# Kernel optimization log

Measured on AMD Instinct MI355X. Metric: run time of the kernel, lower is better.

## Reference

```python
import jax, jax.numpy as jnp
import numpy as np

N = 100000
E = 3200000
NFEAT = 256
NHID = 128
NCLASS = 40
SCALE = 1.0


def setup_inputs() -> dict:
    key = jax.random.key(0)
    ks = jax.random.split(key, 8)
    x = jax.random.normal(ks[0], (N, NFEAT), dtype=jnp.float32)
    adj_row = jnp.sort(jax.random.randint(ks[1], (E,), 0, N, dtype=jnp.int32))
    adj_col = jax.random.randint(ks[2], (E,), 0, N, dtype=jnp.int32)
    adj_val = jax.random.uniform(ks[3], (E,), dtype=jnp.float32)
    # parameters (reset_parameters: weight ~ N(0,1), bias ~ N(-1,1) -> normal with mean -1? no:
    # bias.normal_(-stdv, stdv) with stdv=1 means mean=-1, std=1)
    W1 = jax.random.normal(ks[4], (NFEAT, NHID), dtype=jnp.float32)
    b1 = jax.random.normal(ks[5], (NHID,), dtype=jnp.float32) - 1.0
    W2 = jax.random.normal(ks[6], (NHID, NCLASS), dtype=jnp.float32)
    b2 = jax.random.normal(ks[7], (NCLASS,), dtype=jnp.float32) - 1.0
    return {"x": x, "adj_row": adj_row, "adj_col": adj_col, "adj_val": adj_val,
            "i": 0, "W1": W1, "b1": b1, "W2": W2, "b2": b2}


def spmm(row, col, val, dense):
    # adj @ dense where adj is sparse COO [N, N]
    gathered = val[:, None] * dense[col]          # [E, D]
    return jax.ops.segment_sum(gathered, row, num_segments=N)


def reference(x, adj_row, adj_col, adj_val, i, W1, b1, W2, b2):
    # layer 1: support = x @ W1; out = adj @ support + b1
    h = spmm(adj_row, adj_col, adj_val, x @ W1) + b1
    h = jax.nn.relu(h) * SCALE
    # dropout is identity (eval mode / training=False)
    # layer 2
    logits = spmm(adj_row, adj_col, adj_val, h @ W2) + b2
    return jax.nn.log_softmax(logits, axis=1)
```

## Files before the change

### kernel.cpp

```cpp
#include <hip/hip_runtime.h>
#include <hip/hip_bf16.h>
#include <math.h>


#define GCN_NFEAT 256
#define GCN_NHID  128
#define GCN_NCLASS 40
#define SUP2_LD   64

typedef __bf16 bf16_t;
typedef bf16_t bf16x8 __attribute__((ext_vector_type(8)));
typedef float  f32x4  __attribute__((ext_vector_type(4)));

static __device__ __forceinline__ unsigned short f2b(float f) {
    bf16_t b = (bf16_t)f;
    return *(unsigned short*)&b;
}
static __device__ __forceinline__ float blo(unsigned int u) {
    return __uint_as_float(u << 16);
}
static __device__ __forceinline__ float bhi(unsigned int u) {
    return __uint_as_float(u & 0xffff0000u);
}

__global__ __launch_bounds__(256) void k_row_ptr(
    const int* __restrict__ row, int* __restrict__ row_ptr, int n_rows, int n_edges)
{
    int r = blockIdx.x * blockDim.x + threadIdx.x;
    if (r > n_rows) return;
    int lo = 0, hi = n_edges;
    while (lo < hi) {
        int mid = (lo + hi) >> 1;
        if (row[mid] < r) lo = mid + 1; else hi = mid;
    }
    row_ptr[r] = lo;
}

__global__ __launch_bounds__(256) void k_prep_w1t(
    const float* __restrict__ w1, bf16_t* __restrict__ w1t)
{
    int idx = blockIdx.x * 256 + threadIdx.x;
    int c = idx & 127;
    int k = idx >> 7;
    w1t[(size_t)c * GCN_NFEAT + k] = (bf16_t)w1[(size_t)k * GCN_NHID + c];
}

__global__ __launch_bounds__(256) void k_prep_w2t(
    const float* __restrict__ w2, bf16_t* __restrict__ w2t)
{
    int idx = blockIdx.x * 256 + threadIdx.x;
    if (idx >= 48 * GCN_NHID) return;
    int c = idx / GCN_NHID;
    int k = idx - c * GCN_NHID;
    float v = (c < GCN_NCLASS) ? w2[(size_t)k * GCN_NCLASS + c] : 0.f;
    w2t[idx] = (bf16_t)v;
}

__global__ __launch_bounds__(256) void k_gemm1(
    const float* __restrict__ x, const bf16_t* __restrict__ w1t,
    bf16_t* __restrict__ out, int nrows)
{
    __shared__ __align__(16) bf16_t As[128][72];
    __shared__ __align__(16) bf16_t Bs[128][72];

    const int tid  = threadIdx.x;
    const int wave = tid >> 6, lane = tid & 63;
    const int wm = wave >> 1, wn = wave & 1;
    const int lm = lane & 15, quad = lane >> 4;
    const int r0 = blockIdx.x * 128;

    f32x4 acc[4][4] = {};

    for (int k0 = 0; k0 < GCN_NFEAT; k0 += 64) {
        {
            const int row = tid >> 1, half = tid & 1;
            const int gr = r0 + row;
            union { bf16_t b[32]; uint4 q[4]; } t;
            if (gr < nrows) {
                const float* p = x + (size_t)gr * GCN_NFEAT + k0 + half * 32;
#pragma unroll
                for (int i = 0; i < 8; i++) {
                    float4 v = ((const float4*)p)[i];
                    t.b[i*4+0] = (bf16_t)v.x; t.b[i*4+1] = (bf16_t)v.y;
                    t.b[i*4+2] = (bf16_t)v.z; t.b[i*4+3] = (bf16_t)v.w;
                }
            } else {
#pragma unroll
                for (int i = 0; i < 4; i++) t.q[i] = make_uint4(0,0,0,0);
            }
            uint4* dst = (uint4*)&As[row][half * 32];
#pragma unroll
            for (int i = 0; i < 4; i++) dst[i] = t.q[i];
        }
        {
            const int colc = tid >> 1, half = tid & 1;
            const uint4* src = (const uint4*)(w1t + (size_t)colc * GCN_NFEAT + k0 + half * 32);
            uint4* dst = (uint4*)&Bs[colc][half * 32];
#pragma unroll
            for (int i = 0; i < 4; i++) dst[i] = src[i];
        }
        __syncthreads();

#pragma unroll
        for (int ks = 0; ks < 2; ks++) {
            bf16x8 af[4], bfr[4];
#pragma unroll
            for (int i = 0; i < 4; i++)
                af[i] = *(const bf16x8*)&As[wm*64 + i*16 + lm][ks*32 + quad*8];
#pragma unroll
            for (int j = 0; j < 4; j++)
                bfr[j] = *(const bf16x8*)&Bs[wn*64 + j*16 + lm][ks*32 + quad*8];
#pragma unroll
            for (int i = 0; i < 4; i++)
#pragma unroll
                for (int j = 0; j < 4; j++)
                    acc[i][j] = __builtin_amdgcn_mfma_f32_16x16x32_bf16(
                        af[i], bfr[j], acc[i][j], 0, 0, 0);
        }
        __syncthreads();
    }

#pragma unroll
    for (int i = 0; i < 4; i++) {
#pragma unroll
        for (int reg = 0; reg < 4; reg++) {
            const int gr = r0 + wm*64 + i*16 + quad*4 + reg;
            if (gr < nrows) {
#pragma unroll
                for (int j = 0; j < 4; j++) {
                    const int gc = wn*64 + j*16 + lm;
                    out[(size_t)gr * GCN_NHID + gc] = (bf16_t)acc[i][j][reg];
                }
            }
        }
    }
}

#define S1_FENCE(U) asm volatile("" : "+v"(U.x), "+v"(U.y), "+v"(U.z), "+v"(U.w));
#define S1_FMA(U, V)                                   \
    a0 = fmaf(V, blo(U.x), a0); a1 = fmaf(V, bhi(U.x), a1); \
    a2 = fmaf(V, blo(U.y), a2); a3 = fmaf(V, bhi(U.y), a3); \
    a4 = fmaf(V, blo(U.z), a4); a5 = fmaf(V, bhi(U.z), a5); \
    a6 = fmaf(V, blo(U.w), a6); a7 = fmaf(V, bhi(U.w), a7);

__global__ __launch_bounds__(256) void k_spmm1(
    const int* __restrict__ row_ptr, const int* __restrict__ col,
    const float* __restrict__ val, const bf16_t* __restrict__ sup,
    const float* __restrict__ b1, unsigned int* __restrict__ h, int nrows)
{
    const int wid  = (blockIdx.x * blockDim.x + threadIdx.x) >> 6;
    const int lane = threadIdx.x & 63;
    if (wid >= nrows) return;
    const int q = lane >> 4;
    const int f = lane & 15;
    const int e0 = __builtin_amdgcn_readfirstlane(row_ptr[wid]);
    const int e1 = __builtin_amdgcn_readfirstlane(row_ptr[wid + 1]);
    const int n  = e1 - e0;
    const char* supb = (const char*)sup;
    const int fo = f * 16;

    float a0=0.f,a1=0.f,a2=0.f,a3=0.f,a4=0.f,a5=0.f,a6=0.f,a7=0.f;

    int base = 0;
    for (; base + 16 <= n; base += 16) {
        const int i0 = e0 + base + q;
        const int   c0 = col[i0];      const float v0 = val[i0];
        const int   c1 = col[i0 + 4];  const float v1 = val[i0 + 4];
        const int   c2 = col[i0 + 8];  const float v2 = val[i0 + 8];
        const int   c3 = col[i0 + 12]; const float v3 = val[i0 + 12];
        uint4 u0 = *(const uint4*)(supb + (((size_t)(unsigned)c0) << 8) + fo);
        uint4 u1 = *(const uint4*)(supb + (((size_t)(unsigned)c1) << 8) + fo);
        uint4 u2 = *(const uint4*)(supb + (((size_t)(unsigned)c2) << 8) + fo);
        uint4 u3 = *(const uint4*)(supb + (((size_t)(unsigned)c3) << 8) + fo);
        S1_FENCE(u0) S1_FMA(u0, v0)
        S1_FENCE(u1) S1_FMA(u1, v1)
        S1_FENCE(u2) S1_FMA(u2, v2)
        S1_FENCE(u3) S1_FMA(u3, v3)
    }
    const int rem = n - base;
    if (rem > 0) {
        const int elast = e1 - 1;
        uint4 t0, t1, t2, t3;
        float w0 = 0.f, w1 = 0.f, w2 = 0.f, w3 = 0.f;
        {
            int gi = e0 + base + q; if (gi > elast) gi = elast;
            const int c = col[gi]; w0 = (q < rem) ? val[gi] : 0.f;
            t0 = *(const uint4*)(supb + (((size_t)(unsigned)c) << 8) + fo);
        }
        if (rem > 4) {
            int gi = e0 + base + 4 + q; if (gi > elast) gi = elast;
            const int c = col[gi]; w1 = (4 + q < rem) ? val[gi] : 0.f;
            t1 = *(const uint4*)(supb + (((size_t)(unsigned)c) << 8) + fo);
        }
        if (rem > 8) {
            int gi = e0 + base + 8 + q; if (gi > elast) gi = elast;
            const int c = col[gi]; w2 = (8 + q < rem) ? val[gi] : 0.f;
            t2 = *(const uint4*)(supb + (((size_t)(unsigned)c) << 8) + fo);
        }
        if (rem > 12) {
            int gi = e0 + base + 12 + q; if (gi > elast) gi = elast;
            const int c = col[gi]; w3 = (12 + q < rem) ? val[gi] : 0.f;
            t3 = *(const uint4*)(supb + (((size_t)(unsigned)c) << 8) + fo);
        }
        { S1_FENCE(t0) S1_FMA(t0, w0) }
        if (rem > 4)  { S1_FENCE(t1) S1_FMA(t1, w1) }
        if (rem > 8)  { S1_FENCE(t2) S1_FMA(t2, w2) }
        if (rem > 12) { S1_FENCE(t3) S1_FMA(t3, w3) }
    }

    a0 += __shfl_xor(a0, 16, 64); a1 += __shfl_xor(a1, 16, 64);
    a2 += __shfl_xor(a2, 16, 64); a3 += __shfl_xor(a3, 16, 64);
    a4 += __shfl_xor(a4, 16, 64); a5 += __shfl_xor(a5, 16, 64);
    a6 += __shfl_xor(a6, 16, 64); a7 += __shfl_xor(a7, 16, 64);
    a0 += __shfl_xor(a0, 32, 64); a1 += __shfl_xor(a1, 32, 64);
    a2 += __shfl_xor(a2, 32, 64); a3 += __shfl_xor(a3, 32, 64);
    a4 += __shfl_xor(a4, 32, 64); a5 += __shfl_xor(a5, 32, 64);
    a6 += __shfl_xor(a6, 32, 64); a7 += __shfl_xor(a7, 32, 64);

    if (q == 0) {
        const float4 ba = *(const float4*)(b1 + f * 8);
        const float4 bc = *(const float4*)(b1 + f * 8 + 4);
        const float o0 = fmaxf(a0 + ba.x, 0.f), o1 = fmaxf(a1 + ba.y, 0.f);
        const float o2 = fmaxf(a2 + ba.z, 0.f), o3 = fmaxf(a3 + ba.w, 0.f);
        const float o4 = fmaxf(a4 + bc.x, 0.f), o5 = fmaxf(a5 + bc.y, 0.f);
        const float o6 = fmaxf(a6 + bc.z, 0.f), o7 = fmaxf(a7 + bc.w, 0.f);
        uint4 pk;
        pk.x = (unsigned)f2b(o0) | ((unsigned)f2b(o1) << 16);
        pk.y = (unsigned)f2b(o2) | ((unsigned)f2b(o3) << 16);
        pk.z = (unsigned)f2b(o4) | ((unsigned)f2b(o5) << 16);
        pk.w = (unsigned)f2b(o6) | ((unsigned)f2b(o7) << 16);
        *(uint4*)(h + ((unsigned)wid << 6) + (f << 2)) = pk;
    }
}

__global__ __launch_bounds__(256) void k_gemm2(
    const bf16_t* __restrict__ h, const bf16_t* __restrict__ w2t,
    bf16_t* __restrict__ out, int nrows)
{
    __shared__ __align__(16) bf16_t As[128][136];
    __shared__ __align__(16) bf16_t Bs[48][136];

    const int tid  = threadIdx.x;
    const int wave = tid >> 6, lane = tid & 63;
    const int lm = lane & 15, quad = lane >> 4;
    const int r0 = blockIdx.x * 128;

    {
        const int row = tid >> 1, half = tid & 1;
        const int gr = r0 + row;
        uint4* dst = (uint4*)&As[row][half * 64];
        if (gr < nrows) {
            const uint4* src = (const uint4*)(h + (size_t)gr * GCN_NHID + half * 64);
#pragma unroll
            for (int i = 0; i < 8; i++) dst[i] = src[i];
        } else {
#pragma unroll
            for (int i = 0; i < 8; i++) dst[i] = make_uint4(0,0,0,0);
        }
    }
    for (int idx = tid; idx < 48 * 16; idx += 256) {
        const int c = idx >> 4, seg = idx & 15;
        ((uint4*)&Bs[c][0])[seg] = ((const uint4*)(w2t + (size_t)c * GCN_NHID))[seg];
    }
    __syncthreads();

    f32x4 acc[2][3] = {};
#pragma unroll
    for (int ks = 0; ks < 4; ks++) {
        bf16x8 af[2], bfr[3];
#pragma unroll
        for (int i = 0; i < 2; i++)
            af[i] = *(const bf16x8*)&As[wave*32 + i*16 + lm][ks*32 + quad*8];
#pragma unroll
        for (int j = 0; j < 3; j++)
            bfr[j] = *(const bf16x8*)&Bs[j*16 + lm][ks*32 + quad*8];
#pragma unroll
        for (int i = 0; i < 2; i++)
#pragma unroll
            for (int j = 0; j < 3; j++)
                acc[i][j] = __builtin_amdgcn_mfma_f32_16x16x32_bf16(
                    af[i], bfr[j], acc[i][j], 0, 0, 0);
    }

#pragma unroll
    for (int i = 0; i < 2; i++) {
#pragma unroll
        for (int reg = 0; reg < 4; reg++) {
            const int gr = r0 + wave*32 + i*16 + quad*4 + reg;
            if (gr < nrows) {
#pragma unroll
                for (int j = 0; j < 3; j++) {
                    const int gc = j*16 + lm;
                    out[(size_t)gr * SUP2_LD + gc] = (bf16_t)acc[i][j][reg];
                }
                out[(size_t)gr * SUP2_LD + 48 + lm] = (bf16_t)0.f;
            }
        }
    }
}

#define S2_FENCE(U) asm volatile("" : "+v"(U.x), "+v"(U.y));
#define S2_FMA(U, V)                                   \
    a0 = fmaf(V, blo(U.x), a0); a1 = fmaf(V, bhi(U.x), a1); \
    a2 = fmaf(V, blo(U.y), a2); a3 = fmaf(V, bhi(U.y), a3);

__global__ __launch_bounds__(256) void k_spmm2_lsm(
    const int* __restrict__ row_ptr, const int* __restrict__ col,
    const float* __restrict__ val, const bf16_t* __restrict__ sup2,
    const float* __restrict__ b2, float* __restrict__ out, int nrows)
{
    const int wid  = (blockIdx.x * blockDim.x + threadIdx.x) >> 6;
    const int lane = threadIdx.x & 63;
    if (wid >= nrows) return;
    const int q = lane >> 4;
    const int f = lane & 15;
    const int e0 = __builtin_amdgcn_readfirstlane(row_ptr[wid]);
    const int e1 = __builtin_amdgcn_readfirstlane(row_ptr[wid + 1]);
    const int n  = e1 - e0;
    const char* supb = (const char*)sup2;
    const int fo = f * 8;

    float a0=0.f,a1=0.f,a2=0.f,a3=0.f;

    int base = 0;
    for (; base + 16 <= n; base += 16) {
        const int i0 = e0 + base + q;
        const int   c0 = col[i0];      const float v0 = val[i0];
        const int   c1 = col[i0 + 4];  const float v1 = val[i0 + 4];
        const int   c2 = col[i0 + 8];  const float v2 = val[i0 + 8];
        const int   c3 = col[i0 + 12]; const float v3 = val[i0 + 12];
        uint2 u0 = *(const uint2*)(supb + (((size_t)(unsigned)c0) << 7) + fo);
        uint2 u1 = *(const uint2*)(supb + (((size_t)(unsigned)c1) << 7) + fo);
        uint2 u2 = *(const uint2*)(supb + (((size_t)(unsigned)c2) << 7) + fo);
        uint2 u3 = *(const uint2*)(supb + (((size_t)(unsigned)c3) << 7) + fo);
        S2_FENCE(u0) S2_FMA(u0, v0)
        S2_FENCE(u1) S2_FMA(u1, v1)
        S2_FENCE(u2) S2_FMA(u2, v2)
        S2_FENCE(u3) S2_FMA(u3, v3)
    }
    const int rem = n - base;
    if (rem > 0) {
        const int elast = e1 - 1;
        uint2 t0, t1, t2, t3;
        float w0 = 0.f, w1 = 0.f, w2 = 0.f, w3 = 0.f;
        {
            int gi = e0 + base + q; if (gi > elast) gi = elast;
            const int c = col[gi]; w0 = (q < rem) ? val[gi] : 0.f;
            t0 = *(const uint2*)(supb + (((size_t)(unsigned)c) << 7) + fo);
        }
        if (rem > 4) {
            int gi = e0 + base + 4 + q; if (gi > elast) gi = elast;
            const int c = col[gi]; w1 = (4 + q < rem) ? val[gi] : 0.f;
            t1 = *(const uint2*)(supb + (((size_t)(unsigned)c) << 7) + fo);
        }
        if (rem > 8) {
            int gi = e0 + base + 8 + q; if (gi > elast) gi = elast;
            const int c = col[gi]; w2 = (8 + q < rem) ? val[gi] : 0.f;
            t2 = *(const uint2*)(supb + (((size_t)(unsigned)c) << 7) + fo);
        }
        if (rem > 12) {
            int gi = e0 + base + 12 + q; if (gi > elast) gi = elast;
            const int c = col[gi]; w3 = (12 + q < rem) ? val[gi] : 0.f;
            t3 = *(const uint2*)(supb + (((size_t)(unsigned)c) << 7) + fo);
        }
        { S2_FENCE(t0) S2_FMA(t0, w0) }
        if (rem > 4)  { S2_FENCE(t1) S2_FMA(t1, w1) }
        if (rem > 8)  { S2_FENCE(t2) S2_FMA(t2, w2) }
        if (rem > 12) { S2_FENCE(t3) S2_FMA(t3, w3) }
    }

    a0 += __shfl_xor(a0, 16, 64); a1 += __shfl_xor(a1, 16, 64);
    a2 += __shfl_xor(a2, 16, 64); a3 += __shfl_xor(a3, 16, 64);
    a0 += __shfl_xor(a0, 32, 64); a1 += __shfl_xor(a1, 32, 64);
    a2 += __shfl_xor(a2, 32, 64); a3 += __shfl_xor(a3, 32, 64);

    const bool av = (f < 10);
    float l0 = -INFINITY, l1 = -INFINITY, l2 = -INFINITY, l3 = -INFINITY;
    if (av) {
        const float4 bb = *(const float4*)(b2 + f * 4);
        l0 = a0 + bb.x; l1 = a1 + bb.y; l2 = a2 + bb.z; l3 = a3 + bb.w;
    }
    float m = fmaxf(fmaxf(l0, l1), fmaxf(l2, l3));
    m = fmaxf(m, __shfl_xor(m, 1, 64));
    m = fmaxf(m, __shfl_xor(m, 2, 64));
    m = fmaxf(m, __shfl_xor(m, 4, 64));
    m = fmaxf(m, __shfl_xor(m, 8, 64));
    float s = av ? (__expf(l0 - m) + __expf(l1 - m) + __expf(l2 - m) + __expf(l3 - m)) : 0.f;
    s += __shfl_xor(s, 1, 64);
    s += __shfl_xor(s, 2, 64);
    s += __shfl_xor(s, 4, 64);
    s += __shfl_xor(s, 8, 64);

    if (av && q == 0) {
        const float lse = m + __logf(s);
        float4 o; o.x = l0 - lse; o.y = l1 - lse; o.z = l2 - lse; o.w = l3 - lse;
        *(float4*)(out + (size_t)wid * GCN_NCLASS + f * 4) = o;
    }
}

extern "C" void kernel_launch(void* const* d_in, const int* in_sizes, int n_in,
                              void* d_out, int out_size, void* d_ws, size_t ws_size,
                              hipStream_t stream)
{
    const float* x       = (const float*)d_in[0];
    const int*   adj_row = (const int*)  d_in[1];
    const int*   adj_col = (const int*)  d_in[2];
    const float* adj_val = (const float*)d_in[3];
    const float* W1 = (const float*)d_in[5];
    const float* b1 = (const float*)d_in[6];
    const float* W2 = (const float*)d_in[7];
    const float* b2 = (const float*)d_in[8];
    float* out = (float*)d_out;

    const int N = in_sizes[0] / GCN_NFEAT;
    const int E = in_sizes[1];

    char* ws = (char*)d_ws;
    size_t off = 0;
    int* row_ptr = (int*)(ws + off);
    off += (((size_t)(N + 1) * sizeof(int)) + 1023) & ~(size_t)1023;
    bf16_t* w1t = (bf16_t*)(ws + off);
    off += ((size_t)GCN_NHID * GCN_NFEAT * 2 + 1023) & ~(size_t)1023;
    bf16_t* w2t = (bf16_t*)(ws + off);
    off += ((size_t)48 * GCN_NHID * 2 + 1023) & ~(size_t)1023;
    bf16_t* sup1 = (bf16_t*)(ws + off);
    off += ((size_t)N * GCN_NHID * 2 + 1023) & ~(size_t)1023;
    bf16_t* h = (bf16_t*)(ws + off);
    bf16_t* sup2 = sup1;

    k_row_ptr<<<(N + 1 + 255) / 256, 256, 0, stream>>>(adj_row, row_ptr, N, E);
    k_prep_w1t<<<GCN_NHID * GCN_NFEAT / 256, 256, 0, stream>>>(W1, w1t);
    k_prep_w2t<<<(48 * GCN_NHID + 255) / 256, 256, 0, stream>>>(W2, w2t);
    k_gemm1<<<(N + 127) / 128, 256, 0, stream>>>(x, w1t, sup1, N);
    k_spmm1<<<(N + 3) / 4, 256, 0, stream>>>(row_ptr, adj_col, adj_val,
                                             sup1, b1, (unsigned int*)h, N);
    k_gemm2<<<(N + 127) / 128, 256, 0, stream>>>(h, w2t, sup2, N);
    k_spmm2_lsm<<<(N + 3) / 4, 256, 0, stream>>>(row_ptr, adj_col, adj_val,
                                                 sup2, b2, out, N);
}
```

Before: 392.9 us.

## Fuse spmm1 with gemm2, merge prep kernels, add nontemporal streaming loads

```diff
diff --git a/kernel.cpp b/kernel.cpp
--- a/kernel.cpp
+++ b/kernel.cpp
@@ -11,6 +11,7 @@
 typedef __bf16 bf16_t;
 typedef bf16_t bf16x8 __attribute__((ext_vector_type(8)));
 typedef float  f32x4  __attribute__((ext_vector_type(4)));
+typedef float  f32x4e __attribute__((ext_vector_type(4)));
 
 static __device__ __forceinline__ unsigned short f2b(float f) {
     bf16_t b = (bf16_t)f;
@@ -23,37 +24,35 @@
     return __uint_as_float(u & 0xffff0000u);
 }
 
-__global__ __launch_bounds__(256) void k_row_ptr(
-    const int* __restrict__ row, int* __restrict__ row_ptr, int n_rows, int n_edges)
+__global__ __launch_bounds__(256) void k_prep(
+    const int* __restrict__ row, int* __restrict__ row_ptr,
+    const float* __restrict__ w1, bf16_t* __restrict__ w1t,
+    const float* __restrict__ w2, bf16_t* __restrict__ w2t,
+    int n_rows, int n_edges, int rb)
 {
-    int r = blockIdx.x * blockDim.x + threadIdx.x;
-    if (r > n_rows) return;
-    int lo = 0, hi = n_edges;
-    while (lo < hi) {
-        int mid = (lo + hi) >> 1;
-        if (row[mid] < r) lo = mid + 1; else hi = mid;
-    }
-    row_ptr[r] = lo;
-}
-
-__global__ __launch_bounds__(256) void k_prep_w1t(
-    const float* __restrict__ w1, bf16_t* __restrict__ w1t)
-{
-    int idx = blockIdx.x * 256 + threadIdx.x;
-    int c = idx & 127;
-    int k = idx >> 7;
-    w1t[(size_t)c * GCN_NFEAT + k] = (bf16_t)w1[(size_t)k * GCN_NHID + c];
-}
-
-__global__ __launch_bounds__(256) void k_prep_w2t(
-    const float* __restrict__ w2, bf16_t* __restrict__ w2t)
-{
-    int idx = blockIdx.x * 256 + threadIdx.x;
-    if (idx >= 48 * GCN_NHID) return;
-    int c = idx / GCN_NHID;
-    int k = idx - c * GCN_NHID;
-    float v = (c < GCN_NCLASS) ? w2[(size_t)k * GCN_NCLASS + c] : 0.f;
-    w2t[idx] = (bf16_t)v;
+    const int b = blockIdx.x;
+    if (b < rb) {
+        int r = b * 256 + threadIdx.x;
+        if (r > n_rows) return;
+        int lo = 0, hi = n_edges;
+        while (lo < hi) {
+            int mid = (lo + hi) >> 1;
+            if (row[mid] < r) lo = mid + 1; else hi = mid;
+        }
+        row_ptr[r] = lo;
+    } else if (b < rb + 128) {
+        int idx = (b - rb) * 256 + threadIdx.x;
+        int c = idx & 127;
+        int k = idx >> 7;
+        w1t[(size_t)c * GCN_NFEAT + k] = (bf16_t)w1[(size_t)k * GCN_NHID + c];
+    } else {
+        int idx = (b - rb - 128) * 256 + threadIdx.x;
+        if (idx >= 48 * GCN_NHID) return;
+        int c = idx / GCN_NHID;
+        int k = idx - c * GCN_NHID;
+        float v = (c < GCN_NCLASS) ? w2[(size_t)k * GCN_NCLASS + c] : 0.f;
+        w2t[idx] = (bf16_t)v;
+    }
 }
 
 __global__ __launch_bounds__(256) void k_gemm1(
@@ -77,10 +76,10 @@
             const int gr = r0 + row;
             union { bf16_t b[32]; uint4 q[4]; } t;
             if (gr < nrows) {
-                const float* p = x + (size_t)gr * GCN_NFEAT + k0 + half * 32;
+                const f32x4e* p = (const f32x4e*)(x + (size_t)gr * GCN_NFEAT + k0 + half * 32);
 #pragma unroll
                 for (int i = 0; i < 8; i++) {
-                    float4 v = ((const float4*)p)[i];
+                    f32x4e v = __builtin_nontemporal_load(p + i);
                     t.b[i*4+0] = (bf16_t)v.x; t.b[i*4+1] = (bf16_t)v.y;
                     t.b[i*4+2] = (bf16_t)v.z; t.b[i*4+3] = (bf16_t)v.w;
                 }
@@ -143,98 +142,10 @@
     a4 = fmaf(V, blo(U.z), a4); a5 = fmaf(V, bhi(U.z), a5); \
     a6 = fmaf(V, blo(U.w), a6); a7 = fmaf(V, bhi(U.w), a7);
 
-__global__ __launch_bounds__(256) void k_spmm1(
+__global__ __launch_bounds__(256) void k_spmm1_g2(
     const int* __restrict__ row_ptr, const int* __restrict__ col,
     const float* __restrict__ val, const bf16_t* __restrict__ sup,
-    const float* __restrict__ b1, unsigned int* __restrict__ h, int nrows)
-{
-    const int wid  = (blockIdx.x * blockDim.x + threadIdx.x) >> 6;
-    const int lane = threadIdx.x & 63;
-    if (wid >= nrows) return;
-    const int q = lane >> 4;
-    const int f = lane & 15;
-    const int e0 = __builtin_amdgcn_readfirstlane(row_ptr[wid]);
-    const int e1 = __builtin_amdgcn_readfirstlane(row_ptr[wid + 1]);
-    const int n  = e1 - e0;
-    const char* supb = (const char*)sup;
-    const int fo = f * 16;
-
-    float a0=0.f,a1=0.f,a2=0.f,a3=0.f,a4=0.f,a5=0.f,a6=0.f,a7=0.f;
-
-    int base = 0;
-    for (; base + 16 <= n; base += 16) {
-        const int i0 = e0 + base + q;
-        const int   c0 = col[i0];      const float v0 = val[i0];
-        const int   c1 = col[i0 + 4];  const float v1 = val[i0 + 4];
-        const int   c2 = col[i0 + 8];  const float v2 = val[i0 + 8];
-        const int   c3 = col[i0 + 12]; const float v3 = val[i0 + 12];
-        uint4 u0 = *(const uint4*)(supb + (((size_t)(unsigned)c0) << 8) + fo);
-        uint4 u1 = *(const uint4*)(supb + (((size_t)(unsigned)c1) << 8) + fo);
-        uint4 u2 = *(const uint4*)(supb + (((size_t)(unsigned)c2) << 8) + fo);
-        uint4 u3 = *(const uint4*)(supb + (((size_t)(unsigned)c3) << 8) + fo);
-        S1_FENCE(u0) S1_FMA(u0, v0)
-        S1_FENCE(u1) S1_FMA(u1, v1)
-        S1_FENCE(u2) S1_FMA(u2, v2)
-        S1_FENCE(u3) S1_FMA(u3, v3)
-    }
-    const int rem = n - base;
-    if (rem > 0) {
-        const int elast = e1 - 1;
-        uint4 t0, t1, t2, t3;
-        float w0 = 0.f, w1 = 0.f, w2 = 0.f, w3 = 0.f;
-        {
-            int gi = e0 + base + q; if (gi > elast) gi = elast;
-            const int c = col[gi]; w0 = (q < rem) ? val[gi] : 0.f;
-            t0 = *(const uint4*)(supb + (((size_t)(unsigned)c) << 8) + fo);
-        }
-        if (rem > 4) {
-            int gi = e0 + base + 4 + q; if (gi > elast) gi = elast;
-            const int c = col[gi]; w1 = (4 + q < rem) ? val[gi] : 0.f;
-            t1 = *(const uint4*)(supb + (((size_t)(unsigned)c) << 8) + fo);
-        }
-        if (rem > 8) {
-            int gi = e0 + base + 8 + q; if (gi > elast) gi = elast;
-            const int c = col[gi]; w2 = (8 + q < rem) ? val[gi] : 0.f;
-            t2 = *(const uint4*)(supb + (((size_t)(unsigned)c) << 8) + fo);
-        }
-        if (rem > 12) {
-            int gi = e0 + base + 12 + q; if (gi > elast) gi = elast;
-            const int c = col[gi]; w3 = (12 + q < rem) ? val[gi] : 0.f;
-            t3 = *(const uint4*)(supb + (((size_t)(unsigned)c) << 8) + fo);
-        }
-        { S1_FENCE(t0) S1_FMA(t0, w0) }
-        if (rem > 4)  { S1_FENCE(t1) S1_FMA(t1, w1) }
-        if (rem > 8)  { S1_FENCE(t2) S1_FMA(t2, w2) }
-        if (rem > 12) { S1_FENCE(t3) S1_FMA(t3, w3) }
-    }
-
-    a0 += __shfl_xor(a0, 16, 64); a1 += __shfl_xor(a1, 16, 64);
-    a2 += __shfl_xor(a2, 16, 64); a3 += __shfl_xor(a3, 16, 64);
-    a4 += __shfl_xor(a4, 16, 64); a5 += __shfl_xor(a5, 16, 64);
-    a6 += __shfl_xor(a6, 16, 64); a7 += __shfl_xor(a7, 16, 64);
-    a0 += __shfl_xor(a0, 32, 64); a1 += __shfl_xor(a1, 32, 64);
-    a2 += __shfl_xor(a2, 32, 64); a3 += __shfl_xor(a3, 32, 64);
-    a4 += __shfl_xor(a4, 32, 64); a5 += __shfl_xor(a5, 32, 64);
-    a6 += __shfl_xor(a6, 32, 64); a7 += __shfl_xor(a7, 32, 64);
-
-    if (q == 0) {
-        const float4 ba = *(const float4*)(b1 + f * 8);
-        const float4 bc = *(const float4*)(b1 + f * 8 + 4);
-        const float o0 = fmaxf(a0 + ba.x, 0.f), o1 = fmaxf(a1 + ba.y, 0.f);
-        const float o2 = fmaxf(a2 + ba.z, 0.f), o3 = fmaxf(a3 + ba.w, 0.f);
-        const float o4 = fmaxf(a4 + bc.x, 0.f), o5 = fmaxf(a5 + bc.y, 0.f);
-        const float o6 = fmaxf(a6 + bc.z, 0.f), o7 = fmaxf(a7 + bc.w, 0.f);
-        uint4 pk;
-        pk.x = (unsigned)f2b(o0) | ((unsigned)f2b(o1) << 16);
-        pk.y = (unsigned)f2b(o2) | ((unsigned)f2b(o3) << 16);
-        pk.z = (unsigned)f2b(o4) | ((unsigned)f2b(o5) << 16);
-        pk.w = (unsigned)f2b(o6) | ((unsigned)f2b(o7) << 16);
-        *(uint4*)(h + ((unsigned)wid << 6) + (f << 2)) = pk;
-    }
-}
-
-__global__ __launch_bounds__(256) void k_gemm2(
-    const bf16_t* __restrict__ h, const bf16_t* __restrict__ w2t,
+    const float* __restrict__ b1, const bf16_t* __restrict__ w2t,
     bf16_t* __restrict__ out, int nrows)
 {
     __shared__ __align__(16) bf16_t As[128][136];
@@ -242,28 +153,108 @@
 
     const int tid  = threadIdx.x;
     const int wave = tid >> 6, lane = tid & 63;
-    const int lm = lane & 15, quad = lane >> 4;
+    const int q = lane >> 4;
+    const int f = lane & 15;
     const int r0 = blockIdx.x * 128;
-
-    {
-        const int row = tid >> 1, half = tid & 1;
-        const int gr = r0 + row;
-        uint4* dst = (uint4*)&As[row][half * 64];
-        if (gr < nrows) {
-            const uint4* src = (const uint4*)(h + (size_t)gr * GCN_NHID + half * 64);
-#pragma unroll
-            for (int i = 0; i < 8; i++) dst[i] = src[i];
-        } else {
-#pragma unroll
-            for (int i = 0; i < 8; i++) dst[i] = make_uint4(0,0,0,0);
-        }
-    }
+    const char* supb = (const char*)sup;
+    const int fo = f * 16;
+
     for (int idx = tid; idx < 48 * 16; idx += 256) {
         const int c = idx >> 4, seg = idx & 15;
         ((uint4*)&Bs[c][0])[seg] = ((const uint4*)(w2t + (size_t)c * GCN_NHID))[seg];
     }
+
+    const float4 ba = *(const float4*)(b1 + f * 8);
+    const float4 bc = *(const float4*)(b1 + f * 8 + 4);
+
+    int e1next = -1;
+    for (int i = 0; i < 32; i++) {
+        const int r = r0 + wave * 32 + i;
+        if (r >= nrows) break;
+        const int e0 = (e1next >= 0) ? e1next
+                                     : __builtin_amdgcn_readfirstlane(row_ptr[r]);
+        const int e1 = __builtin_amdgcn_readfirstlane(row_ptr[r + 1]);
+        e1next = e1;
+        const int n = e1 - e0;
+
+        float a0=0.f,a1=0.f,a2=0.f,a3=0.f,a4=0.f,a5=0.f,a6=0.f,a7=0.f;
+
+        int base = 0;
+        for (; base + 16 <= n; base += 16) {
+            const int i0 = e0 + base + q;
+            const int   c0 = __builtin_nontemporal_load(col + i0);
+            const float v0 = __builtin_nontemporal_load(val + i0);
+            const int   c1 = __builtin_nontemporal_load(col + i0 + 4);
+            const float v1 = __builtin_nontemporal_load(val + i0 + 4);
+            const int   c2 = __builtin_nontemporal_load(col + i0 + 8);
+            const float v2 = __builtin_nontemporal_load(val + i0 + 8);
+            const int   c3 = __builtin_nontemporal_load(col + i0 + 12);
+            const float v3 = __builtin_nontemporal_load(val + i0 + 12);
+            uint4 u0 = *(const uint4*)(supb + (((size_t)(unsigned)c0) << 8) + fo);
+            uint4 u1 = *(const uint4*)(supb + (((size_t)(unsigned)c1) << 8) + fo);
+            uint4 u2 = *(const uint4*)(supb + (((size_t)(unsigned)c2) << 8) + fo);
+            uint4 u3 = *(const uint4*)(supb + (((size_t)(unsigned)c3) << 8) + fo);
+            S1_FENCE(u0) S1_FMA(u0, v0)
+            S1_FENCE(u1) S1_FMA(u1, v1)
+            S1_FENCE(u2) S1_FMA(u2, v2)
+            S1_FENCE(u3) S1_FMA(u3, v3)
+        }
+        const int rem = n - base;
+        if (rem > 0) {
+            const int elast = e1 - 1;
+            uint4 t0, t1, t2, t3;
+            float w0 = 0.f, w1 = 0.f, w2 = 0.f, w3 = 0.f;
+            {
+                int gi = e0 + base + q; if (gi > elast) gi = elast;
+                const int c = col[gi]; w0 = (q < rem) ? val[gi] : 0.f;
+                t0 = *(const uint4*)(supb + (((size_t)(unsigned)c) << 8) + fo);
+            }
+            if (rem > 4) {
+                int gi = e0 + base + 4 + q; if (gi > elast) gi = elast;
+                const int c = col[gi]; w1 = (4 + q < rem) ? val[gi] : 0.f;
+                t1 = *(const uint4*)(supb + (((size_t)(unsigned)c) << 8) + fo);
+            }
+            if (rem > 8) {
+                int gi = e0 + base + 8 + q; if (gi > elast) gi = elast;
+                const int c = col[gi]; w2 = (8 + q < rem) ? val[gi] : 0.f;
+                t2 = *(const uint4*)(supb + (((size_t)(unsigned)c) << 8) + fo);
+            }
+            if (rem > 12) {
+                int gi = e0 + base + 12 + q; if (gi > elast) gi = elast;
+                const int c = col[gi]; w3 = (12 + q < rem) ? val[gi] : 0.f;
+                t3 = *(const uint4*)(supb + (((size_t)(unsigned)c) << 8) + fo);
+            }
+            { S1_FENCE(t0) S1_FMA(t0, w0) }
+            if (rem > 4)  { S1_FENCE(t1) S1_FMA(t1, w1) }
+            if (rem > 8)  { S1_FENCE(t2) S1_FMA(t2, w2) }
+            if (rem > 12) { S1_FENCE(t3) S1_FMA(t3, w3) }
+        }
+
+        a0 += __shfl_xor(a0, 16, 64); a1 += __shfl_xor(a1, 16, 64);
+        a2 += __shfl_xor(a2, 16, 64); a3 += __shfl_xor(a3, 16, 64);
+        a4 += __shfl_xor(a4, 16, 64); a5 += __shfl_xor(a5, 16, 64);
+        a6 += __shfl_xor(a6, 16, 64); a7 += __shfl_xor(a7, 16, 64);
+        a0 += __shfl_xor(a0, 32, 64); a1 += __shfl_xor(a1, 32, 64);
+        a2 += __shfl_xor(a2, 32, 64); a3 += __shfl_xor(a3, 32, 64);
+        a4 += __shfl_xor(a4, 32, 64); a5 += __shfl_xor(a5, 32, 64);
+        a6 += __shfl_xor(a6, 32, 64); a7 += __shfl_xor(a7, 32, 64);
+
+        if (q == 0) {
+            const float o0 = fmaxf(a0 + ba.x, 0.f), o1 = fmaxf(a1 + ba.y, 0.f);
+            const float o2 = fmaxf(a2 + ba.z, 0.f), o3 = fmaxf(a3 + ba.w, 0.f);
+            const float o4 = fmaxf(a4 + bc.x, 0.f), o5 = fmaxf(a5 + bc.y, 0.f);
+            const float o6 = fmaxf(a6 + bc.z, 0.f), o7 = fmaxf(a7 + bc.w, 0.f);
+            uint4 pk;
+            pk.x = (unsigned)f2b(o0) | ((unsigned)f2b(o1) << 16);
+            pk.y = (unsigned)f2b(o2) | ((unsigned)f2b(o3) << 16);
+            pk.z = (unsigned)f2b(o4) | ((unsigned)f2b(o5) << 16);
+            pk.w = (unsigned)f2b(o6) | ((unsigned)f2b(o7) << 16);
+            *(uint4*)&As[wave * 32 + i][f * 8] = pk;
+        }
+    }
     __syncthreads();
 
+    const int lm = lane & 15, quad = lane >> 4;
     f32x4 acc[2][3] = {};
 #pragma unroll
     for (int ks = 0; ks < 4; ks++) {
@@ -293,7 +284,6 @@
                     const int gc = j*16 + lm;
                     out[(size_t)gr * SUP2_LD + gc] = (bf16_t)acc[i][j][reg];
                 }
-                out[(size_t)gr * SUP2_LD + 48 + lm] = (bf16_t)0.f;
             }
         }
     }
@@ -325,10 +315,14 @@
     int base = 0;
     for (; base + 16 <= n; base += 16) {
         const int i0 = e0 + base + q;
-        const int   c0 = col[i0];      const float v0 = val[i0];
-        const int   c1 = col[i0 + 4];  const float v1 = val[i0 + 4];
-        const int   c2 = col[i0 + 8];  const float v2 = val[i0 + 8];
-        const int   c3 = col[i0 + 12]; const float v3 = val[i0 + 12];
+        const int   c0 = __builtin_nontemporal_load(col + i0);
+        const float v0 = __builtin_nontemporal_load(val + i0);
+        const int   c1 = __builtin_nontemporal_load(col + i0 + 4);
+        const float v1 = __builtin_nontemporal_load(val + i0 + 4);
+        const int   c2 = __builtin_nontemporal_load(col + i0 + 8);
+        const float v2 = __builtin_nontemporal_load(val + i0 + 8);
+        const int   c3 = __builtin_nontemporal_load(col + i0 + 12);
+        const float v3 = __builtin_nontemporal_load(val + i0 + 12);
         uint2 u0 = *(const uint2*)(supb + (((size_t)(unsigned)c0) << 7) + fo);
         uint2 u1 = *(const uint2*)(supb + (((size_t)(unsigned)c1) << 7) + fo);
         uint2 u2 = *(const uint2*)(supb + (((size_t)(unsigned)c2) << 7) + fo);
@@ -393,8 +387,10 @@
 
     if (av && q == 0) {
         const float lse = m + __logf(s);
-        float4 o; o.x = l0 - lse; o.y = l1 - lse; o.z = l2 - lse; o.w = l3 - lse;
-        *(float4*)(out + (size_t)wid * GCN_NCLASS + f * 4) = o;
+        f32x4e o;
+        o.x = l0 - lse; o.y = l1 - lse; o.z = l2 - lse; o.w = l3 - lse;
+        f32x4e* p = (f32x4e*)(out + (size_t)wid * GCN_NCLASS + f * 4);
+        __builtin_nontemporal_store(o, p);
     }
 }
 
@@ -425,16 +421,14 @@
     off += ((size_t)48 * GCN_NHID * 2 + 1023) & ~(size_t)1023;
     bf16_t* sup1 = (bf16_t*)(ws + off);
     off += ((size_t)N * GCN_NHID * 2 + 1023) & ~(size_t)1023;
-    bf16_t* h = (bf16_t*)(ws + off);
-    bf16_t* sup2 = sup1;
-
-    k_row_ptr<<<(N + 1 + 255) / 256, 256, 0, stream>>>(adj_row, row_ptr, N, E);
-    k_prep_w1t<<<GCN_NHID * GCN_NFEAT / 256, 256, 0, stream>>>(W1, w1t);
-    k_prep_w2t<<<(48 * GCN_NHID + 255) / 256, 256, 0, stream>>>(W2, w2t);
+    bf16_t* sup2 = (bf16_t*)(ws + off);
+
+    const int rb = (N + 1 + 255) / 256;
+    k_prep<<<rb + 128 + 24, 256, 0, stream>>>(adj_row, row_ptr, W1, w1t, W2, w2t,
+                                              N, E, rb);
     k_gemm1<<<(N + 127) / 128, 256, 0, stream>>>(x, w1t, sup1, N);
-    k_spmm1<<<(N + 3) / 4, 256, 0, stream>>>(row_ptr, adj_col, adj_val,
-                                             sup1, b1, (unsigned int*)h, N);
-    k_gemm2<<<(N + 127) / 128, 256, 0, stream>>>(h, w2t, sup2, N);
+    k_spmm1_g2<<<(N + 127) / 128, 256, 0, stream>>>(row_ptr, adj_col, adj_val,
+                                                    sup1, b1, w2t, sup2, N);
     k_spmm2_lsm<<<(N + 3) / 4, 256, 0, stream>>>(row_ptr, adj_col, adj_val,
                                                  sup2, b2, out, N);
 }
```

Measured after the change: 529.1 us. 1.35x slower.
